# Kernel optimization log

Hardware: AMD Instinct MI355X
Metric: run time of the kernel (lower is better)

## Reference

```python
import jax, jax.numpy as jnp
import numpy as np

B, S, D, H = 2, 2048, 1024, 16
HD = D // H  # head_dim = 64


def setup_inputs() -> dict:
    key = jax.random.key(0)
    ks = jax.random.split(key, 12)
    s = 1.0 / np.sqrt(D)
    return {
        "query": jax.random.normal(ks[0], (B, S, D), jnp.float32),
        "key": jax.random.normal(ks[1], (B, S, D), jnp.float32),
        "value": jax.random.normal(ks[2], (B, S, D), jnp.float32),
        "attention_mask": jnp.zeros((B, S, S), jnp.float32),
        "WQ_w": jax.random.normal(ks[3], (D, D), jnp.float32) * s,
        "WQ_b": jnp.zeros((D,), jnp.float32),
        "WK_w": jax.random.normal(ks[4], (D, D), jnp.float32) * s,
        "WK_b": jnp.zeros((D,), jnp.float32),
        "WV_w": jax.random.normal(ks[5], (D, D), jnp.float32) * s,
        "WV_b": jnp.zeros((D,), jnp.float32),
        "WO_w": jax.random.normal(ks[6], (D, D), jnp.float32) * s,
        "WO_b": jnp.zeros((D,), jnp.float32),
    }


def _split_heads(x):
    # [B,S,D] -> [B,H,S,HD]
    b, s, _ = x.shape
    return x.reshape(b, s, H, HD).transpose(0, 2, 1, 3)


def reference(query, key, value, attention_mask,
              WQ_w, WQ_b, WK_w, WK_b, WV_w, WV_b, WO_w, WO_b):
    Q = _split_heads(query @ WQ_w.T + WQ_b)   # [B,H,S,HD]
    K = _split_heads(key @ WK_w.T + WK_b)
    V = _split_heads(value @ WV_w.T + WV_b)
    scale = 1.0 / jnp.sqrt(jnp.float32(HD))
    scores = jnp.einsum('bhqd,bhkd->bhqk', Q, K) * scale
    scores = scores + attention_mask[:, None, :, :]
    attn = jax.nn.softmax(scores, axis=-1)    # dropout_prob=0.0 -> identity
    out = jnp.einsum('bhqk,bhkd->bhqd', attn, V)
    out = out.transpose(0, 2, 1, 3).reshape(query.shape[0], -1, D)
    return out @ WO_w.T + WO_b
```

## Files before the change

kernel.cpp:

```cpp
#include <hip/hip_runtime.h>
#include <math.h>


typedef _Float16 h8 __attribute__((ext_vector_type(8)));
typedef _Float16 h4 __attribute__((ext_vector_type(4)));
typedef float f4 __attribute__((ext_vector_type(4)));

#define MFMA16(a, b, c) __builtin_amdgcn_mfma_f32_16x16x32_f16((a), (b), (c), 0, 0, 0)
#define EXP2F(x) __builtin_amdgcn_exp2f(x)

static constexpr int Bn = 2, Sn = 2048, Dn = 1024, Hn = 16, HDn = 64;
static constexpr int Mn = Bn * Sn;
static constexpr int Kn = Dn;
static constexpr int Nn = Dn;
static constexpr int LDP = 72;
static constexpr float LOG2E = 1.4426950408889634f;

__device__ __forceinline__ void gload_lds16(const _Float16* g, _Float16* l) {
  __builtin_amdgcn_global_load_lds(
      (const __attribute__((address_space(1))) unsigned int*)g,
      (__attribute__((address_space(3))) unsigned int*)l, 16, 0, 0);
}

struct CvtJobs {
  const float* src[7];
  _Float16* dst[7];
  int n4[7];
};

__global__ __launch_bounds__(256) void cvt_kernel(CvtJobs j) {
  const int stride = gridDim.x * blockDim.x;
  const int t0 = blockIdx.x * blockDim.x + threadIdx.x;
#pragma unroll
  for (int k = 0; k < 7; ++k) {
    const float4* __restrict__ s = (const float4*)j.src[k];
    h4* __restrict__ d = (h4*)j.dst[k];
    const int n = j.n4[k];
    for (int i = t0; i < n; i += stride) {
      const float4 f = s[i];
      h4 h;
      h[0] = (_Float16)f.x; h[1] = (_Float16)f.y;
      h[2] = (_Float16)f.z; h[3] = (_Float16)f.w;
      d[i] = h;
    }
  }
}

__global__ __launch_bounds__(256) void cvt_mask(const float* __restrict__ src,
                                                _Float16* __restrict__ dst, int n4) {
  const int stride = gridDim.x * blockDim.x;
  const float4* __restrict__ s = (const float4*)src;
  h4* __restrict__ d = (h4*)dst;
  for (int i = blockIdx.x * blockDim.x + threadIdx.x; i < n4; i += stride) {
    const float4 f = s[i];
    h4 h;
    h[0] = (_Float16)(f.x * LOG2E); h[1] = (_Float16)(f.y * LOG2E);
    h[2] = (_Float16)(f.z * LOG2E); h[3] = (_Float16)(f.w * LOG2E);
    d[i] = h;
  }
}

struct QkvArgs {
  const _Float16* X[3];
  const _Float16* W[3];
  const float* bias[3];
  _Float16* out[3];
};

__global__ __launch_bounds__(256) void gemm_qkv(QkvArgs args) {
  const int z = blockIdx.z;
  const _Float16* __restrict__ X = args.X[z];
  const _Float16* __restrict__ W = args.W[z];
  const float* __restrict__ bias = args.bias[z];
  _Float16* __restrict__ out = args.out[z];

  __shared__ _Float16 As[128 * 64];
  __shared__ _Float16 Bs[128 * 64];

  const int t = threadIdx.x;
  const int lane = t & 63, wv = t >> 6;
  const int l15 = lane & 15, quad = lane >> 4;
  const int wm = (wv >> 1) * 64, wn = (wv & 1) * 64;
  const int n0 = blockIdx.x * 128, m0 = blockIdx.y * 128;

  f4 acc[4][4];
#pragma unroll
  for (int i = 0; i < 4; ++i)
#pragma unroll
    for (int j = 0; j < 4; ++j) {
      f4 zz = {0.f, 0.f, 0.f, 0.f};
      acc[i][j] = zz;
    }

  const int srow = lane >> 3, scol = (lane & 7) * 8;

  for (int k0 = 0; k0 < Kn; k0 += 64) {
    __syncthreads();
#pragma unroll
    for (int u = 0; u < 4; ++u) {
      const int s = wv * 4 + u;
      const int row = s * 8 + srow;
      gload_lds16(X + (size_t)(m0 + row) * Kn + k0 + scol, As + s * 512);
      gload_lds16(W + (size_t)(n0 + row) * Kn + k0 + scol, Bs + s * 512);
    }
    __syncthreads();
#pragma unroll
    for (int kk = 0; kk < 64; kk += 32) {
      h8 af[4], bfr[4];
#pragma unroll
      for (int i = 0; i < 4; ++i)
        af[i] = *(const h8*)&As[(wm + i * 16 + l15) * 64 + kk + quad * 8];
#pragma unroll
      for (int j = 0; j < 4; ++j)
        bfr[j] = *(const h8*)&Bs[(wn + j * 16 + l15) * 64 + kk + quad * 8];
#pragma unroll
      for (int i = 0; i < 4; ++i)
#pragma unroll
        for (int j = 0; j < 4; ++j)
          acc[i][j] = MFMA16(af[i], bfr[j], acc[i][j]);
    }
  }

  const float osc = (z == 0) ? (0.125f * LOG2E) : 1.0f;
  if (z != 2) {
#pragma unroll
    for (int j = 0; j < 4; ++j) {
      const int n = n0 + wn + j * 16 + l15;
      const float bvs = bias[n] * osc;
      const int hh = n >> 6, hd = n & 63;
#pragma unroll
      for (int i = 0; i < 4; ++i) {
        const int mb = m0 + wm + i * 16 + quad * 4;
        const int bb = mb >> 11;
#pragma unroll
        for (int r = 0; r < 4; ++r) {
          const int ss = (mb + r) & (Sn - 1);
          out[(((size_t)(bb * Hn + hh)) * Sn + ss) * HDn + hd] =
              (_Float16)(acc[i][j][r] * osc + bvs);
        }
      }
    }
  } else {
#pragma unroll
    for (int j = 0; j < 4; ++j) {
      const int n = n0 + wn + j * 16 + l15;
      const float bv = bias[n];
      const int hh = n >> 6, hd = n & 63;
#pragma unroll
      for (int i = 0; i < 4; ++i) {
        const int mb = m0 + wm + i * 16 + quad * 4;
        const int bb = mb >> 11, ss = mb & (Sn - 1);
        h4 hv;
#pragma unroll
        for (int r = 0; r < 4; ++r) hv[r] = (_Float16)(acc[i][j][r] + bv);
        *(h4*)(out + (((size_t)(bb * Hn + hh)) * HDn + hd) * Sn + ss) = hv;
      }
    }
  }
}

__global__ __launch_bounds__(256) void gemm_o(const _Float16* __restrict__ X,
                                              const _Float16* __restrict__ W,
                                              const float* __restrict__ bias,
                                              float* __restrict__ out) {
  __shared__ _Float16 As[128 * 64];
  __shared__ _Float16 Bs[128 * 64];

  const int t = threadIdx.x;
  const int lane = t & 63, wv = t >> 6;
  const int l15 = lane & 15, quad = lane >> 4;
  const int wm = (wv >> 1) * 64, wn = (wv & 1) * 64;
  const int n0 = blockIdx.x * 128, m0 = blockIdx.y * 128;

  f4 acc[4][4];
#pragma unroll
  for (int i = 0; i < 4; ++i)
#pragma unroll
    for (int j = 0; j < 4; ++j) {
      f4 zz = {0.f, 0.f, 0.f, 0.f};
      acc[i][j] = zz;
    }

  const int srow = lane >> 3, scol = (lane & 7) * 8;

  for (int k0 = 0; k0 < Kn; k0 += 64) {
    __syncthreads();
#pragma unroll
    for (int u = 0; u < 4; ++u) {
      const int s = wv * 4 + u;
      const int row = s * 8 + srow;
      gload_lds16(X + (size_t)(m0 + row) * Kn + k0 + scol, As + s * 512);
      gload_lds16(W + (size_t)(n0 + row) * Kn + k0 + scol, Bs + s * 512);
    }
    __syncthreads();
#pragma unroll
    for (int kk = 0; kk < 64; kk += 32) {
      h8 af[4], bfr[4];
#pragma unroll
      for (int i = 0; i < 4; ++i)
        af[i] = *(const h8*)&As[(wm + i * 16 + l15) * 64 + kk + quad * 8];
#pragma unroll
      for (int j = 0; j < 4; ++j)
        bfr[j] = *(const h8*)&Bs[(wn + j * 16 + l15) * 64 + kk + quad * 8];
#pragma unroll
      for (int i = 0; i < 4; ++i)
#pragma unroll
        for (int j = 0; j < 4; ++j)
          acc[i][j] = MFMA16(af[i], bfr[j], acc[i][j]);
    }
  }

#pragma unroll
  for (int j = 0; j < 4; ++j) {
    const int n = n0 + wn + j * 16 + l15;
    const float bv = bias[n];
#pragma unroll
    for (int i = 0; i < 4; ++i) {
      const int mb = m0 + wm + i * 16 + quad * 4;
#pragma unroll
      for (int r = 0; r < 4; ++r)
        out[(size_t)(mb + r) * Nn + n] = acc[i][j][r] + bv;
    }
  }
}

__global__ __launch_bounds__(512) void attn_kernel(
    const _Float16* __restrict__ Qh,
    const _Float16* __restrict__ Kh,
    const _Float16* __restrict__ Vt,
    const _Float16* __restrict__ maskh,
    _Float16* __restrict__ out) {
  __shared__ _Float16 smem[4 * 64 * LDP];

  const int t = threadIdx.x;
  const int w = t >> 6, lane = t & 63;
  const int l15 = lane & 15, quad = lane >> 4;
  const int g = w >> 2;
  const int wq = w & 3;

  const int bh = blockIdx.y;
  const int b = bh >> 4, h = bh & 15;
  const size_t headoff = (size_t)bh * Sn * HDn;
  const _Float16* Qp = Qh + headoff;
  const _Float16* Kp = Kh + headoff;
  const _Float16* Vp = Vt + headoff;

  const int qb = blockIdx.x * 64;
  const int q0 = qb + wq * 16;
  const h8 qf0 = *(const h8*)(Qp + (size_t)(q0 + l15) * HDn + quad * 8);
  const h8 qf1 = *(const h8*)(Qp + (size_t)(q0 + l15) * HDn + 32 + quad * 8);

  const int kbase = g * (Sn / 2);
  const _Float16* mrow = maskh + ((size_t)b * Sn + q0 + l15) * Sn + kbase;

  float m_run = -INFINITY, l_part = 0.f;
  f4 o_acc[4];
#pragma unroll
  for (int nt = 0; nt < 4; ++nt) {
    f4 zz = {0.f, 0.f, 0.f, 0.f};
    o_acc[nt] = zz;
  }

  _Float16* Kg = smem + g * (64 * LDP);
  _Float16* Vg = smem + (2 + g) * (64 * LDP);

  const int tg = t & 255;
  const int srow = tg >> 3, sc8 = (tg & 7) * 8;
  const int srow1 = srow + 32;
  const int a = tg & 7;
  const int vb = ((a >> 2) & 1) * 32 + (a & 1) * 16 + ((a >> 1) & 1) * 4;

  constexpr int NT = (Sn / 2) / 64;

  uint4 kreg0, kreg1, vreg0, vreg1;
  uint2 mreg[4];
  auto kv_issue = [&](int kt) {
    kreg0 = *(const uint4*)(Kp + (size_t)(kbase + kt * 64 + srow) * HDn + sc8);
    vreg0 = *(const uint4*)(Vp + (size_t)srow * Sn + kbase + kt * 64 + sc8);
    kreg1 = *(const uint4*)(Kp + (size_t)(kbase + kt * 64 + srow1) * HDn + sc8);
    vreg1 = *(const uint4*)(Vp + (size_t)srow1 * Sn + kbase + kt * 64 + sc8);
  };
  auto m_issue = [&](int kt) {
#pragma unroll
    for (int ks = 0; ks < 4; ++ks)
      mreg[ks] = *(const uint2*)(mrow + kt * 64 + ks * 16 + quad * 4);
  };

  kv_issue(0);
  m_issue(0);

  for (int kt = 0; kt < NT; ++kt) {
    __syncthreads();
    *(uint4*)&Kg[srow * LDP + sc8] = kreg0;
    *(uint4*)&Kg[srow1 * LDP + sc8] = kreg1;
    *(uint2*)&Vg[srow * LDP + vb] = make_uint2(vreg0.x, vreg0.y);
    *(uint2*)&Vg[srow * LDP + vb + 8] = make_uint2(vreg0.z, vreg0.w);
    *(uint2*)&Vg[srow1 * LDP + vb] = make_uint2(vreg1.x, vreg1.y);
    *(uint2*)&Vg[srow1 * LDP + vb + 8] = make_uint2(vreg1.z, vreg1.w);
    __syncthreads();
    const int nx = (kt + 1 < NT) ? kt + 1 : kt;
    kv_issue(nx);

    f4 s[4];
#pragma unroll
    for (int ks = 0; ks < 4; ++ks) {
      const h4 mh = *(const h4*)&mreg[ks];
      f4 acc0;
#pragma unroll
      for (int r = 0; r < 4; ++r) acc0[r] = (float)mh[r];
      const h8 kf0 = *(const h8*)&Kg[(ks * 16 + l15) * LDP + quad * 8];
      const h8 kf1 = *(const h8*)&Kg[(ks * 16 + l15) * LDP + 32 + quad * 8];
      acc0 = MFMA16(kf0, qf0, acc0);
      s[ks] = MFMA16(kf1, qf1, acc0);
    }
    m_issue(nx);

    float mx = s[0][0];
#pragma unroll
    for (int ks = 0; ks < 4; ++ks)
#pragma unroll
      for (int r = 0; r < 4; ++r) mx = fmaxf(mx, s[ks][r]);
    mx = fmaxf(mx, __shfl_xor(mx, 16));
    mx = fmaxf(mx, __shfl_xor(mx, 32));
    if (!__all(mx - m_run <= 8.0f)) {
      const float nm = fmaxf(m_run, mx);
      const float alpha = EXP2F(m_run - nm);
      m_run = nm;
      l_part *= alpha;
#pragma unroll
      for (int nt = 0; nt < 4; ++nt)
#pragma unroll
        for (int r = 0; r < 4; ++r) o_acc[nt][r] *= alpha;
    }
    float sm = 0.f;
#pragma unroll
    for (int ks = 0; ks < 4; ++ks)
#pragma unroll
      for (int r = 0; r < 4; ++r) {
        s[ks][r] = EXP2F(s[ks][r] - m_run);
        sm += s[ks][r];
      }
    l_part += sm;

#pragma unroll
    for (int c = 0; c < 2; ++c) {
      h8 pf;
#pragma unroll
      for (int r = 0; r < 4; ++r) pf[r] = (_Float16)s[2 * c][r];
#pragma unroll
      for (int r = 0; r < 4; ++r) pf[4 + r] = (_Float16)s[2 * c + 1][r];
#pragma unroll
      for (int nt = 0; nt < 4; ++nt) {
        const h8 vf = *(const h8*)&Vg[(nt * 16 + l15) * LDP + c * 32 + quad * 8];
        o_acc[nt] = MFMA16(vf, pf, o_acc[nt]);
      }
    }
  }

  l_part += __shfl_xor(l_part, 16);
  l_part += __shfl_xor(l_part, 32);

  __syncthreads();
  float* Uex = (float*)smem;
  float* mex = Uex + 4 * 16 * LDP;
  float* lex = mex + 64;
  if (g == 1) {
#pragma unroll
    for (int nt = 0; nt < 4; ++nt)
      *(f4*)&Uex[wq * 16 * LDP + l15 * LDP + nt * 16 + quad * 4] = o_acc[nt];
    if (quad == 0) {
      mex[wq * 16 + l15] = m_run;
      lex[wq * 16 + l15] = l_part;
    }
  }
  __syncthreads();
  if (g == 0) {
    const float m1 = mex[wq * 16 + l15];
    const float l1 = lex[wq * 16 + l15];
    const float mm = fmaxf(m_run, m1);
    const float f0 = EXP2F(m_run - mm);
    const float f1 = EXP2F(m1 - mm);
    const float rl = 1.0f / (f0 * l_part + f1 * l1);
    _Float16* Ob = smem + 3 * (64 * LDP) + (w * 16) * LDP;
#pragma unroll
    for (int nt = 0; nt < 4; ++nt) {
      const f4 Ur = *(const f4*)&Uex[wq * 16 * LDP + l15 * LDP + nt * 16 + quad * 4];
      h4 ov;
#pragma unroll
      for (int r = 0; r < 4; ++r)
        ov[r] = (_Float16)((o_acc[nt][r] * f0 + Ur[r] * f1) * rl);
      *(h4*)&Ob[l15 * LDP + nt * 16 + quad * 4] = ov;
    }
    const int qr = lane >> 2;
    const int seg = (lane & 3) * 16;
    _Float16* dst = out + ((size_t)b * Sn + q0 + qr) * Dn + h * 64 + seg;
    *(uint4*)dst = *(const uint4*)&Ob[qr * LDP + seg];
    *(uint4*)(dst + 8) = *(const uint4*)&Ob[qr * LDP + seg + 8];
  }
}

extern "C" void kernel_launch(void* const* d_in, const int* in_sizes, int n_in,
                              void* d_out, int out_size, void* d_ws, size_t ws_size,
                              hipStream_t stream) {
  const float* q = (const float*)d_in[0];
  const float* k = (const float*)d_in[1];
  const float* v = (const float*)d_in[2];
  const float* mask = (const float*)d_in[3];
  const float* WQ = (const float*)d_in[4];
  const float* bQ = (const float*)d_in[5];
  const float* WK = (const float*)d_in[6];
  const float* bK = (const float*)d_in[7];
  const float* WV = (const float*)d_in[8];
  const float* bV = (const float*)d_in[9];
  const float* WO = (const float*)d_in[10];
  const float* bO = (const float*)d_in[11];

  _Float16* ws = (_Float16*)d_ws;
  const size_t MD = (size_t)Mn * Dn;
  const size_t DD = (size_t)Dn * Dn;
  _Float16* qh  = ws;
  _Float16* kh  = ws + MD;
  _Float16* vh  = ws + 2 * MD;
  _Float16* WQh = ws + 3 * MD;
  _Float16* WKh = WQh + DD;
  _Float16* WVh = WKh + DD;
  _Float16* WOh = WVh + DD;
  _Float16* Qh  = ws + 3 * MD + 4 * DD;
  _Float16* Kh  = Qh + MD;
  _Float16* Vt  = Kh + MD;
  _Float16* AO  = qh;
  _Float16* Mh  = kh;

  CvtJobs cj;
  cj.src[0] = q;  cj.dst[0] = qh;  cj.n4[0] = (int)(MD / 4);
  cj.src[1] = k;  cj.dst[1] = kh;  cj.n4[1] = (int)(MD / 4);
  cj.src[2] = v;  cj.dst[2] = vh;  cj.n4[2] = (int)(MD / 4);
  cj.src[3] = WQ; cj.dst[3] = WQh; cj.n4[3] = (int)(DD / 4);
  cj.src[4] = WK; cj.dst[4] = WKh; cj.n4[4] = (int)(DD / 4);
  cj.src[5] = WV; cj.dst[5] = WVh; cj.n4[5] = (int)(DD / 4);
  cj.src[6] = WO; cj.dst[6] = WOh; cj.n4[6] = (int)(DD / 4);
  cvt_kernel<<<1024, 256, 0, stream>>>(cj);

  QkvArgs ga;
  ga.X[0] = qh; ga.W[0] = WQh; ga.bias[0] = bQ; ga.out[0] = Qh;
  ga.X[1] = kh; ga.W[1] = WKh; ga.bias[1] = bK; ga.out[1] = Kh;
  ga.X[2] = vh; ga.W[2] = WVh; ga.bias[2] = bV; ga.out[2] = Vt;
  gemm_qkv<<<dim3(Nn / 128, Mn / 128, 3), 256, 0, stream>>>(ga);

  cvt_mask<<<2048, 256, 0, stream>>>(mask, Mh, (int)((size_t)Bn * Sn * Sn / 4));

  attn_kernel<<<dim3(Sn / 64, Bn * Hn), 512, 0, stream>>>(Qh, Kh, Vt, Mh, AO);

  gemm_o<<<dim3(Nn / 128, Mn / 128), 256, 0, stream>>>(AO, WOh, bO, (float*)d_out);
}
```

Measured before the change: 305.4 us.

## Fold mask conversion into input cvt kernel and remap attention blocks per XCD

```diff
diff --git a/kernel.cpp b/kernel.cpp
--- a/kernel.cpp
+++ b/kernel.cpp
@@ -23,40 +23,28 @@
 }
 
 struct CvtJobs {
-  const float* src[7];
-  _Float16* dst[7];
-  int n4[7];
+  const float* src[8];
+  _Float16* dst[8];
+  int n4[8];
+  float scl[8];
 };
 
 __global__ __launch_bounds__(256) void cvt_kernel(CvtJobs j) {
   const int stride = gridDim.x * blockDim.x;
   const int t0 = blockIdx.x * blockDim.x + threadIdx.x;
 #pragma unroll
-  for (int k = 0; k < 7; ++k) {
+  for (int k = 0; k < 8; ++k) {
     const float4* __restrict__ s = (const float4*)j.src[k];
     h4* __restrict__ d = (h4*)j.dst[k];
     const int n = j.n4[k];
+    const float sc = j.scl[k];
     for (int i = t0; i < n; i += stride) {
       const float4 f = s[i];
       h4 h;
-      h[0] = (_Float16)f.x; h[1] = (_Float16)f.y;
-      h[2] = (_Float16)f.z; h[3] = (_Float16)f.w;
+      h[0] = (_Float16)(f.x * sc); h[1] = (_Float16)(f.y * sc);
+      h[2] = (_Float16)(f.z * sc); h[3] = (_Float16)(f.w * sc);
       d[i] = h;
     }
-  }
-}
-
-__global__ __launch_bounds__(256) void cvt_mask(const float* __restrict__ src,
-                                                _Float16* __restrict__ dst, int n4) {
-  const int stride = gridDim.x * blockDim.x;
-  const float4* __restrict__ s = (const float4*)src;
-  h4* __restrict__ d = (h4*)dst;
-  for (int i = blockIdx.x * blockDim.x + threadIdx.x; i < n4; i += stride) {
-    const float4 f = s[i];
-    h4 h;
-    h[0] = (_Float16)(f.x * LOG2E); h[1] = (_Float16)(f.y * LOG2E);
-    h[2] = (_Float16)(f.z * LOG2E); h[3] = (_Float16)(f.w * LOG2E);
-    d[i] = h;
   }
 }
 
@@ -238,14 +226,18 @@
   const int g = w >> 2;
   const int wq = w & 3;
 
-  const int bh = blockIdx.y;
+  const int bid = blockIdx.y * gridDim.x + blockIdx.x;
+  const int xcd = bid & 7;
+  const int idx = bid >> 3;
+  const int bh = (xcd << 2) | (idx >> 5);
+  const int qb = (idx & 31) * 64;
+
   const int b = bh >> 4, h = bh & 15;
   const size_t headoff = (size_t)bh * Sn * HDn;
   const _Float16* Qp = Qh + headoff;
   const _Float16* Kp = Kh + headoff;
   const _Float16* Vp = Vt + headoff;
 
-  const int qb = blockIdx.x * 64;
   const int q0 = qb + wq * 16;
   const h8 qf0 = *(const h8*)(Qp + (size_t)(q0 + l15) * HDn + quad * 8);
   const h8 qf1 = *(const h8*)(Qp + (size_t)(q0 + l15) * HDn + 32 + quad * 8);
@@ -418,6 +410,7 @@
   _Float16* ws = (_Float16*)d_ws;
   const size_t MD = (size_t)Mn * Dn;
   const size_t DD = (size_t)Dn * Dn;
+  const size_t SS = (size_t)Bn * Sn * Sn;
   _Float16* qh  = ws;
   _Float16* kh  = ws + MD;
   _Float16* vh  = ws + 2 * MD;
@@ -429,16 +422,20 @@
   _Float16* Kh  = Qh + MD;
   _Float16* Vt  = Kh + MD;
   _Float16* AO  = qh;
-  _Float16* Mh  = kh;
+  const size_t used = 6 * MD + 4 * DD;
+  _Float16* Mh = (ws_size >= (used + SS) * sizeof(_Float16))
+                     ? (ws + used)
+                     : (_Float16*)d_out;
 
   CvtJobs cj;
-  cj.src[0] = q;  cj.dst[0] = qh;  cj.n4[0] = (int)(MD / 4);
-  cj.src[1] = k;  cj.dst[1] = kh;  cj.n4[1] = (int)(MD / 4);
-  cj.src[2] = v;  cj.dst[2] = vh;  cj.n4[2] = (int)(MD / 4);
-  cj.src[3] = WQ; cj.dst[3] = WQh; cj.n4[3] = (int)(DD / 4);
-  cj.src[4] = WK; cj.dst[4] = WKh; cj.n4[4] = (int)(DD / 4);
-  cj.src[5] = WV; cj.dst[5] = WVh; cj.n4[5] = (int)(DD / 4);
-  cj.src[6] = WO; cj.dst[6] = WOh; cj.n4[6] = (int)(DD / 4);
+  cj.src[0] = q;    cj.dst[0] = qh;  cj.n4[0] = (int)(MD / 4);  cj.scl[0] = 1.f;
+  cj.src[1] = k;    cj.dst[1] = kh;  cj.n4[1] = (int)(MD / 4);  cj.scl[1] = 1.f;
+  cj.src[2] = v;    cj.dst[2] = vh;  cj.n4[2] = (int)(MD / 4);  cj.scl[2] = 1.f;
+  cj.src[3] = WQ;   cj.dst[3] = WQh; cj.n4[3] = (int)(DD / 4);  cj.scl[3] = 1.f;
+  cj.src[4] = WK;   cj.dst[4] = WKh; cj.n4[4] = (int)(DD / 4);  cj.scl[4] = 1.f;
+  cj.src[5] = WV;   cj.dst[5] = WVh; cj.n4[5] = (int)(DD / 4);  cj.scl[5] = 1.f;
+  cj.src[6] = WO;   cj.dst[6] = WOh; cj.n4[6] = (int)(DD / 4);  cj.scl[6] = 1.f;
+  cj.src[7] = mask; cj.dst[7] = Mh;  cj.n4[7] = (int)(SS / 4);  cj.scl[7] = LOG2E;
   cvt_kernel<<<1024, 256, 0, stream>>>(cj);
 
   QkvArgs ga;
@@ -447,8 +444,6 @@
   ga.X[2] = vh; ga.W[2] = WVh; ga.bias[2] = bV; ga.out[2] = Vt;
   gemm_qkv<<<dim3(Nn / 128, Mn / 128, 3), 256, 0, stream>>>(ga);
 
-  cvt_mask<<<2048, 256, 0, stream>>>(mask, Mh, (int)((size_t)Bn * Sn * Sn / 4));
-
   attn_kernel<<<dim3(Sn / 64, Bn * Hn), 512, 0, stream>>>(Qh, Kh, Vt, Mh, AO);
 
   gemm_o<<<dim3(Nn / 128, Mn / 128), 256, 0, stream>>>(AO, WOh, bO, (float*)d_out);
```

Measured after the change: 305.0 us. No clear change (-0.1%).
